# Performance work log

Hardware: AMD Instinct MI355X
Metric: run time of the kernel (lower is better)

Reference implementation:

```python
import jax, jax.numpy as jnp
import numpy as np

N_NODES = 50000
N_EDGES = 600000
IN_FEATS = 128
N_HIDDEN = 128
N_CLASSES = 64


def setup_inputs() -> dict:
    key = jax.random.key(0)
    ks = jax.random.split(key, 10)
    x = jax.random.normal(ks[0], (N_NODES, IN_FEATS), dtype=jnp.float32)
    w = jax.random.uniform(ks[1], (N_EDGES,), dtype=jnp.float32)
    src = jax.random.randint(ks[2], (N_EDGES,), 0, N_NODES, dtype=jnp.int32)
    dst = jax.random.randint(ks[3], (N_EDGES,), 0, N_NODES, dtype=jnp.int32)
    W1 = jax.random.normal(ks[4], (IN_FEATS, N_HIDDEN), dtype=jnp.float32) * 0.05
    b1 = jnp.zeros((N_HIDDEN,), dtype=jnp.float32)
    W2 = jax.random.normal(ks[5], (N_HIDDEN, N_HIDDEN), dtype=jnp.float32) * 0.05
    b2 = jnp.zeros((N_HIDDEN,), dtype=jnp.float32)
    W3 = jax.random.normal(ks[6], (N_HIDDEN, N_CLASSES), dtype=jnp.float32) * 0.05
    b3 = jnp.zeros((N_CLASSES,), dtype=jnp.float32)
    return {"x": x, "w": w, "src": src, "dst": dst,
            "W1": W1, "b1": b1, "W2": W2, "b2": b2, "W3": W3, "b3": b3}


def _graph_conv(h, Wl, bl, w, src, dst, n_nodes):
    # dense linear transform
    h = h @ Wl + bl  # [N, d_out]
    # u_mul_e: gather source features, scale by edge weight
    m = h[src] * w[:, None]  # [E, d_out]
    # sum aggregation into destination nodes
    return jax.ops.segment_sum(m, dst, num_segments=n_nodes)  # [N, d_out]


def reference(x, w, src, dst, W1, b1, W2, b2, W3, b3):
    n = x.shape[0]
    h = jax.nn.relu(_graph_conv(x, W1, b1, w, src, dst, n))
    h = jax.nn.relu(_graph_conv(h, W2, b2, w, src, dst, n))
    return _graph_conv(h, W3, b3, w, src, dst, n)
```

## Files before the change

### kernel.cpp

```cpp
#include <hip/hip_runtime.h>


typedef __attribute__((ext_vector_type(8))) short short8;
typedef __attribute__((ext_vector_type(4))) float float4v;

constexpr int CAP  = 48;
constexpr int CPAD = 16;

__device__ inline unsigned bf16_rne(float f) {
    unsigned u = __float_as_uint(f);
    return (u + 0x7FFF + ((u >> 16) & 1)) >> 16;
}
__device__ inline float bf_lo(unsigned t) { return __uint_as_float(t << 16); }
__device__ inline float bf_hi(unsigned t) { return __uint_as_float(t & 0xFFFF0000u); }

__device__ inline void wprep_one(const float* __restrict__ Wm, int M, int tt,
                                 unsigned short* __restrict__ WfH,
                                 unsigned short* __restrict__ WfL) {
    const int FT = M / 16;
    int lane = tt & 63;
    int ft   = (tt >> 6) % FT;
    int ks   = tt / (64 * FT);
    int n     = ft * 16 + (lane & 15);
    int kbase = ks * 32 + (lane >> 4) * 8;
    #pragma unroll
    for (int j = 0; j < 8; j++) {
        float wv = Wm[(size_t)(kbase + j) * M + n];
        unsigned hb = bf16_rne(wv);
        float wh = __uint_as_float(hb << 16);
        unsigned lb = bf16_rne(wv - wh);
        WfH[(size_t)tt * 8 + j] = (unsigned short)hb;
        WfL[(size_t)tt * 8 + j] = (unsigned short)lb;
    }
}

__global__ void prep_kernel(const float* __restrict__ W1, const float* __restrict__ W2,
                            const float* __restrict__ W3,
                            unsigned short* WfH1, unsigned short* WfL1,
                            unsigned short* WfH2, unsigned short* WfL2,
                            unsigned short* WfH3, unsigned short* WfL3,
                            int* __restrict__ countsP, int N) {
    int t = blockIdx.x * blockDim.x + threadIdx.x;
    if (t < 2048)       wprep_one(W1, 128, t,        WfH1, WfL1);
    else if (t < 4096)  wprep_one(W2, 128, t - 2048, WfH2, WfL2);
    else if (t < 5120)  wprep_one(W3,  64, t - 4096, WfH3, WfL3);
    const int total = N * CPAD;
    for (int i = t; i < total; i += gridDim.x * blockDim.x) countsP[i] = 0;
}

__global__ void scatter_v5(const int* __restrict__ src, const int* __restrict__ dst,
                           const float* __restrict__ w, int* __restrict__ countsP,
                           int2* __restrict__ erec, int E) {
    int e = (blockIdx.x * blockDim.x + threadIdx.x) * 4;
    if (e + 3 < E) {
        int4   d4 = *(const int4*)(dst + e);
        int4   s4 = *(const int4*)(src + e);
        float4 w4 = *(const float4*)(w + e);
        int p0 = atomicAdd(&countsP[d4.x * CPAD], 1);
        int p1 = atomicAdd(&countsP[d4.y * CPAD], 1);
        int p2 = atomicAdd(&countsP[d4.z * CPAD], 1);
        int p3 = atomicAdd(&countsP[d4.w * CPAD], 1);
        if (p0 < CAP) erec[(size_t)d4.x * CAP + p0] = (int2){s4.x, __float_as_int(w4.x)};
        if (p1 < CAP) erec[(size_t)d4.y * CAP + p1] = (int2){s4.y, __float_as_int(w4.y)};
        if (p2 < CAP) erec[(size_t)d4.z * CAP + p2] = (int2){s4.z, __float_as_int(w4.z)};
        if (p3 < CAP) erec[(size_t)d4.w * CAP + p3] = (int2){s4.w, __float_as_int(w4.w)};
    } else {
        for (; e < E; e++) {
            int d = dst[e];
            int p = atomicAdd(&countsP[d * CPAD], 1);
            if (p < CAP) erec[(size_t)d * CAP + p] = (int2){src[e], __float_as_int(w[e])};
        }
    }
}

template <int M>
__global__ __launch_bounds__(256) void gemm_kernel(const float* __restrict__ H,
                                                   const unsigned short* __restrict__ WfH,
                                                   const unsigned short* __restrict__ WfL,
                                                   const float* __restrict__ bias,
                                                   unsigned short* __restrict__ T, int N) {
    const int K  = 128;
    const int KP = K + 4;
    const int FT = M / 16;
    __shared__ float Hs[64 * KP];

    const int node0 = blockIdx.x * 64;
    for (int i = threadIdx.x; i < 64 * (K / 4); i += 256) {
        int r = i / (K / 4), c = i % (K / 4);
        int node = node0 + r;
        float4 hv = {0, 0, 0, 0};
        if (node < N) hv = ((const float4*)(H + (size_t)node * K))[c];
        *(float4*)(Hs + r * KP + c * 4) = hv;
    }
    __syncthreads();

    const int wave = threadIdx.x >> 6;
    const int lane = threadIdx.x & 63;
    const int row  = lane & 15;
    const int ksub = (lane >> 4) * 8;
    const float* hrow = Hs + (wave * 16 + row) * KP;

    float4v acc[FT];
    #pragma unroll
    for (int ft = 0; ft < FT; ft++) acc[ft] = (float4v){0.f, 0.f, 0.f, 0.f};

    #pragma unroll
    for (int ks = 0; ks < 4; ks++) {
        const float* ap = hrow + ks * 32 + ksub;
        float4 a0 = *(const float4*)(ap);
        float4 a1 = *(const float4*)(ap + 4);
        float av[8] = {a0.x, a0.y, a0.z, a0.w, a1.x, a1.y, a1.z, a1.w};
        short8 ah, al;
        #pragma unroll
        for (int j = 0; j < 8; j++) {
            unsigned hb = bf16_rne(av[j]);
            float fh = __uint_as_float(hb << 16);
            ah[j] = (short)hb;
            al[j] = (short)bf16_rne(av[j] - fh);
        }
        #pragma unroll
        for (int ft = 0; ft < FT; ft++) {
            short8 bh = *(const short8*)(WfH + ((size_t)(ks * FT + ft) * 64 + lane) * 8);
            short8 bl = *(const short8*)(WfL + ((size_t)(ks * FT + ft) * 64 + lane) * 8);
            acc[ft] = __builtin_amdgcn_mfma_f32_16x16x32_bf16(ah, bh, acc[ft], 0, 0, 0);
            acc[ft] = __builtin_amdgcn_mfma_f32_16x16x32_bf16(al, bh, acc[ft], 0, 0, 0);
            acc[ft] = __builtin_amdgcn_mfma_f32_16x16x32_bf16(ah, bl, acc[ft], 0, 0, 0);
        }
    }

    const int col   = lane & 15;
    const int rbase = (lane >> 4) * 4;
    #pragma unroll
    for (int ft = 0; ft < FT; ft++) {
        int feat = ft * 16 + col;
        float bv = bias[feat];
        #pragma unroll
        for (int r = 0; r < 4; r++) {
            int node = node0 + wave * 16 + rbase + r;
            if (node < N)
                T[(size_t)node * M + feat] = (unsigned short)bf16_rne(acc[ft][r] + bv);
        }
    }
}

template <int M>
__global__ __launch_bounds__(256) void gemm_bf_kernel(const unsigned short* __restrict__ Hb,
                                                      const unsigned short* __restrict__ WfH,
                                                      const unsigned short* __restrict__ WfL,
                                                      const float* __restrict__ bias,
                                                      unsigned short* __restrict__ T, int N) {
    const int FT = M / 16;
    const int wave = threadIdx.x >> 6;
    const int lane = threadIdx.x & 63;
    const int row  = lane & 15;
    const int ksub = (lane >> 4) * 8;
    const int node0 = blockIdx.x * 64;
    int nodeA = node0 + wave * 16 + row;
    const unsigned short* hp = Hb + (size_t)(nodeA < N ? nodeA : N - 1) * 128;

    float4v acc[FT];
    #pragma unroll
    for (int ft = 0; ft < FT; ft++) acc[ft] = (float4v){0.f, 0.f, 0.f, 0.f};

    #pragma unroll
    for (int ks = 0; ks < 4; ks++) {
        short8 ah = *(const short8*)(hp + ks * 32 + ksub);
        #pragma unroll
        for (int ft = 0; ft < FT; ft++) {
            short8 bh = *(const short8*)(WfH + ((size_t)(ks * FT + ft) * 64 + lane) * 8);
            short8 bl = *(const short8*)(WfL + ((size_t)(ks * FT + ft) * 64 + lane) * 8);
            acc[ft] = __builtin_amdgcn_mfma_f32_16x16x32_bf16(ah, bh, acc[ft], 0, 0, 0);
            acc[ft] = __builtin_amdgcn_mfma_f32_16x16x32_bf16(ah, bl, acc[ft], 0, 0, 0);
        }
    }

    const int col   = lane & 15;
    const int rbase = (lane >> 4) * 4;
    #pragma unroll
    for (int ft = 0; ft < FT; ft++) {
        int feat = ft * 16 + col;
        float bv = bias[feat];
        #pragma unroll
        for (int r = 0; r < 4; r++) {
            int node = node0 + wave * 16 + rbase + r;
            if (node < N)
                T[(size_t)node * M + feat] = (unsigned short)bf16_rne(acc[ft][r] + bv);
        }
    }
}

__global__ void agg128_bf(const unsigned short* __restrict__ Tin,
                          const int* __restrict__ countsP,
                          const int2* __restrict__ erec,
                          unsigned short* __restrict__ Hb, int N) {
    const int wid  = threadIdx.x >> 6;
    const int lane = threadIdx.x & 63;
    const int v = blockIdx.x * 4 + wid;
    if (v >= N) return;
    const int c = min(countsP[v * CPAD], CAP);
    const int q  = lane >> 4;
    const int fo = (lane & 15) * 8;
    float a0 = 0, a1 = 0, a2 = 0, a3 = 0, a4 = 0, a5 = 0, a6 = 0, a7 = 0;
    if (c > 0) {
        const int2* eb = erec + (size_t)v * CAP;
        for (int i = 0; i < c; i += 16) {
            #pragma unroll
            for (int u = 0; u < 4; u++) {
                int idx = i + u * 4 + q;
                float wv = 0.f;
                int cl = idx < c ? idx : c - 1;
                int2 r = eb[cl];
                if (idx < c) wv = __int_as_float(r.y);
                uint4 t = *(const uint4*)(Tin + (size_t)r.x * 128 + fo);
                a0 = fmaf(wv, bf_lo(t.x), a0); a1 = fmaf(wv, bf_hi(t.x), a1);
                a2 = fmaf(wv, bf_lo(t.y), a2); a3 = fmaf(wv, bf_hi(t.y), a3);
                a4 = fmaf(wv, bf_lo(t.z), a4); a5 = fmaf(wv, bf_hi(t.z), a5);
                a6 = fmaf(wv, bf_lo(t.w), a6); a7 = fmaf(wv, bf_hi(t.w), a7);
            }
        }
        a0 += __shfl_xor(a0, 32); a1 += __shfl_xor(a1, 32);
        a2 += __shfl_xor(a2, 32); a3 += __shfl_xor(a3, 32);
        a4 += __shfl_xor(a4, 32); a5 += __shfl_xor(a5, 32);
        a6 += __shfl_xor(a6, 32); a7 += __shfl_xor(a7, 32);
        a0 += __shfl_xor(a0, 16); a1 += __shfl_xor(a1, 16);
        a2 += __shfl_xor(a2, 16); a3 += __shfl_xor(a3, 16);
        a4 += __shfl_xor(a4, 16); a5 += __shfl_xor(a5, 16);
        a6 += __shfl_xor(a6, 16); a7 += __shfl_xor(a7, 16);
    }
    if (lane < 16) {
        float av[8] = {fmaxf(a0, 0.f), fmaxf(a1, 0.f), fmaxf(a2, 0.f), fmaxf(a3, 0.f),
                       fmaxf(a4, 0.f), fmaxf(a5, 0.f), fmaxf(a6, 0.f), fmaxf(a7, 0.f)};
        short8 o;
        #pragma unroll
        for (int j = 0; j < 8; j++) o[j] = (short)bf16_rne(av[j]);
        *(short8*)(Hb + (size_t)v * 128 + fo) = o;
    }
}

__global__ void agg_final_v4(const unsigned short* __restrict__ Tin,
                             const int* __restrict__ countsP,
                             const int2* __restrict__ erec,
                             float* __restrict__ OUT, int N) {
    const int wid  = threadIdx.x >> 6;
    const int lane = threadIdx.x & 63;
    const int v = blockIdx.x * 4 + wid;
    if (v >= N) return;
    const int c = min(countsP[v * CPAD], CAP);
    const int o8 = lane >> 3;
    const int fo = (lane & 7) * 8;
    float a0 = 0, a1 = 0, a2 = 0, a3 = 0, a4 = 0, a5 = 0, a6 = 0, a7 = 0;
    if (c > 0) {
        const int2* eb = erec + (size_t)v * CAP;
        for (int i = 0; i < c; i += 16) {
            #pragma unroll
            for (int u = 0; u < 2; u++) {
                int idx = i + u * 8 + o8;
                float wv = 0.f;
                int cl = idx < c ? idx : c - 1;
                int2 r = eb[cl];
                if (idx < c) wv = __int_as_float(r.y);
                uint4 t = *(const uint4*)(Tin + (size_t)r.x * 64 + fo);
                a0 = fmaf(wv, bf_lo(t.x), a0); a1 = fmaf(wv, bf_hi(t.x), a1);
                a2 = fmaf(wv, bf_lo(t.y), a2); a3 = fmaf(wv, bf_hi(t.y), a3);
                a4 = fmaf(wv, bf_lo(t.z), a4); a5 = fmaf(wv, bf_hi(t.z), a5);
                a6 = fmaf(wv, bf_lo(t.w), a6); a7 = fmaf(wv, bf_hi(t.w), a7);
            }
        }
        a0 += __shfl_xor(a0, 32); a1 += __shfl_xor(a1, 32);
        a2 += __shfl_xor(a2, 32); a3 += __shfl_xor(a3, 32);
        a4 += __shfl_xor(a4, 32); a5 += __shfl_xor(a5, 32);
        a6 += __shfl_xor(a6, 32); a7 += __shfl_xor(a7, 32);
        a0 += __shfl_xor(a0, 16); a1 += __shfl_xor(a1, 16);
        a2 += __shfl_xor(a2, 16); a3 += __shfl_xor(a3, 16);
        a4 += __shfl_xor(a4, 16); a5 += __shfl_xor(a5, 16);
        a6 += __shfl_xor(a6, 16); a7 += __shfl_xor(a7, 16);
        a0 += __shfl_xor(a0, 8);  a1 += __shfl_xor(a1, 8);
        a2 += __shfl_xor(a2, 8);  a3 += __shfl_xor(a3, 8);
        a4 += __shfl_xor(a4, 8);  a5 += __shfl_xor(a5, 8);
        a6 += __shfl_xor(a6, 8);  a7 += __shfl_xor(a7, 8);
    }
    if (lane < 8) {
        float4 o0 = {a0, a1, a2, a3};
        float4 o1 = {a4, a5, a6, a7};
        float* op = OUT + (size_t)v * 64 + fo;
        *(float4*)(op)     = o0;
        *(float4*)(op + 4) = o1;
    }
}

extern "C" void kernel_launch(void* const* d_in, const int* in_sizes, int n_in,
                              void* d_out, int out_size, void* d_ws, size_t ws_size,
                              hipStream_t stream) {
    const float* x   = (const float*)d_in[0];
    const float* w   = (const float*)d_in[1];
    const int*   src = (const int*)d_in[2];
    const int*   dst = (const int*)d_in[3];
    const float* W1  = (const float*)d_in[4];
    const float* b1  = (const float*)d_in[5];
    const float* W2  = (const float*)d_in[6];
    const float* b2  = (const float*)d_in[7];
    const float* W3  = (const float*)d_in[8];
    const float* b3  = (const float*)d_in[9];
    const int N = in_sizes[0] / 128;
    const int E = in_sizes[1];

    unsigned short* Tbf  = (unsigned short*)d_ws;
    unsigned short* Hbf  = Tbf + (size_t)N * 128;
    int2* erec     = (int2*)(Hbf + (size_t)N * 128);
    int*  countsP  = (int*)(erec + (size_t)N * CAP);
    size_t off = (size_t)(countsP + (size_t)N * CPAD - (int*)d_ws);
    off = (off + 3) & ~(size_t)3;
    unsigned short* WfH1 = (unsigned short*)((int*)d_ws + off);
    unsigned short* WfL1 = WfH1 + 128 * 128;
    unsigned short* WfH2 = WfL1 + 128 * 128;
    unsigned short* WfL2 = WfH2 + 128 * 128;
    unsigned short* WfH3 = WfL2 + 128 * 128;
    unsigned short* WfL3 = WfH3 + 128 * 64;

    const int GB = (N + 63) / 64;
    const int AB = (N + 3) / 4;

    prep_kernel<<<96, 256, 0, stream>>>(W1, W2, W3, WfH1, WfL1, WfH2, WfL2,
                                        WfH3, WfL3, countsP, N);
    gemm_kernel<128><<<GB, 256, 0, stream>>>(x, WfH1, WfL1, b1, Tbf, N);
    scatter_v5<<<(E / 4 + 255) / 256, 256, 0, stream>>>(src, dst, w, countsP, erec, E);
    agg128_bf<<<AB, 256, 0, stream>>>(Tbf, countsP, erec, Hbf, N);
    gemm_bf_kernel<128><<<GB, 256, 0, stream>>>(Hbf, WfH2, WfL2, b2, Tbf, N);
    agg128_bf<<<AB, 256, 0, stream>>>(Tbf, countsP, erec, Hbf, N);
    gemm_bf_kernel<64><<<GB, 256, 0, stream>>>(Hbf, WfH3, WfL3, b3, Tbf, N);
    agg_final_v4<<<AB, 256, 0, stream>>>(Tbf, countsP, erec, (float*)d_out, N);
}
```

Before: 242.0 us.

## Fuse edge scatter into layer-1 GEMM launch and prefetch edge records in aggregation

Merges the edge-bucketing scatter and the first dense GEMM into one launch, with the first SB blocks doing the scatter and the rest doing the GEMM, so the two independent stages overlap and one launch is saved. The aggregation kernels now load the first batch of edge records before reading the count and prefetch the next batch during accumulation, so the gather no longer waits on the record load. The count-zeroing loop only clears the used slot of each padded counter. Prefetching reads padded slots past the count that are never used, and the fused kernel mixes two very different block workloads.

After: 236.5 us. 2.3% less time.

```diff
diff --git a/kernel.cpp b/kernel.cpp
--- a/kernel.cpp
+++ b/kernel.cpp
@@ -44,47 +44,47 @@
     if (t < 2048)       wprep_one(W1, 128, t,        WfH1, WfL1);
     else if (t < 4096)  wprep_one(W2, 128, t - 2048, WfH2, WfL2);
     else if (t < 5120)  wprep_one(W3,  64, t - 4096, WfH3, WfL3);
-    const int total = N * CPAD;
-    for (int i = t; i < total; i += gridDim.x * blockDim.x) countsP[i] = 0;
-}
-
-__global__ void scatter_v5(const int* __restrict__ src, const int* __restrict__ dst,
-                           const float* __restrict__ w, int* __restrict__ countsP,
-                           int2* __restrict__ erec, int E) {
-    int e = (blockIdx.x * blockDim.x + threadIdx.x) * 4;
-    if (e + 3 < E) {
-        int4   d4 = *(const int4*)(dst + e);
-        int4   s4 = *(const int4*)(src + e);
-        float4 w4 = *(const float4*)(w + e);
-        int p0 = atomicAdd(&countsP[d4.x * CPAD], 1);
-        int p1 = atomicAdd(&countsP[d4.y * CPAD], 1);
-        int p2 = atomicAdd(&countsP[d4.z * CPAD], 1);
-        int p3 = atomicAdd(&countsP[d4.w * CPAD], 1);
-        if (p0 < CAP) erec[(size_t)d4.x * CAP + p0] = (int2){s4.x, __float_as_int(w4.x)};
-        if (p1 < CAP) erec[(size_t)d4.y * CAP + p1] = (int2){s4.y, __float_as_int(w4.y)};
-        if (p2 < CAP) erec[(size_t)d4.z * CAP + p2] = (int2){s4.z, __float_as_int(w4.z)};
-        if (p3 < CAP) erec[(size_t)d4.w * CAP + p3] = (int2){s4.w, __float_as_int(w4.w)};
-    } else {
-        for (; e < E; e++) {
-            int d = dst[e];
-            int p = atomicAdd(&countsP[d * CPAD], 1);
-            if (p < CAP) erec[(size_t)d * CAP + p] = (int2){src[e], __float_as_int(w[e])};
-        }
-    }
-}
-
-template <int M>
-__global__ __launch_bounds__(256) void gemm_kernel(const float* __restrict__ H,
-                                                   const unsigned short* __restrict__ WfH,
-                                                   const unsigned short* __restrict__ WfL,
-                                                   const float* __restrict__ bias,
-                                                   unsigned short* __restrict__ T, int N) {
+    for (int i = t; i < N; i += gridDim.x * blockDim.x) countsP[i * CPAD] = 0;
+}
+
+__global__ __launch_bounds__(256) void l1_fused(
+        const float* __restrict__ H,
+        const unsigned short* __restrict__ WfH, const unsigned short* __restrict__ WfL,
+        const float* __restrict__ bias, unsigned short* __restrict__ T,
+        const int* __restrict__ src, const int* __restrict__ dst,
+        const float* __restrict__ w, int* __restrict__ countsP,
+        int2* __restrict__ erec, int N, int E, int SB) {
     const int K  = 128;
     const int KP = K + 4;
+    const int M  = 128;
     const int FT = M / 16;
     __shared__ float Hs[64 * KP];
 
-    const int node0 = blockIdx.x * 64;
+    if ((int)blockIdx.x < SB) {
+        int e = (blockIdx.x * 256 + threadIdx.x) * 4;
+        if (e + 3 < E) {
+            int4   d4 = *(const int4*)(dst + e);
+            int4   s4 = *(const int4*)(src + e);
+            float4 w4 = *(const float4*)(w + e);
+            int p0 = atomicAdd(&countsP[d4.x * CPAD], 1);
+            int p1 = atomicAdd(&countsP[d4.y * CPAD], 1);
+            int p2 = atomicAdd(&countsP[d4.z * CPAD], 1);
+            int p3 = atomicAdd(&countsP[d4.w * CPAD], 1);
+            if (p0 < CAP) erec[(size_t)d4.x * CAP + p0] = (int2){s4.x, __float_as_int(w4.x)};
+            if (p1 < CAP) erec[(size_t)d4.y * CAP + p1] = (int2){s4.y, __float_as_int(w4.y)};
+            if (p2 < CAP) erec[(size_t)d4.z * CAP + p2] = (int2){s4.z, __float_as_int(w4.z)};
+            if (p3 < CAP) erec[(size_t)d4.w * CAP + p3] = (int2){s4.w, __float_as_int(w4.w)};
+        } else {
+            for (; e < E; e++) {
+                int d = dst[e];
+                int p = atomicAdd(&countsP[d * CPAD], 1);
+                if (p < CAP) erec[(size_t)d * CAP + p] = (int2){src[e], __float_as_int(w[e])};
+            }
+        }
+        return;
+    }
+
+    const int node0 = (blockIdx.x - SB) * 64;
     for (int i = threadIdx.x; i < 64 * (K / 4); i += 256) {
         int r = i / (K / 4), c = i % (K / 4);
         int node = node0 + r;
@@ -197,36 +197,48 @@
     const int lane = threadIdx.x & 63;
     const int v = blockIdx.x * 4 + wid;
     if (v >= N) return;
-    const int c = min(countsP[v * CPAD], CAP);
     const int q  = lane >> 4;
     const int fo = (lane & 15) * 8;
+    const int2* eb = erec + (size_t)v * CAP;
+
+    int   rx[4]; float wv[4];
+    #pragma unroll
+    for (int u = 0; u < 4; u++) {
+        int2 r = eb[u * 4 + q];
+        rx[u] = r.x; wv[u] = __int_as_float(r.y);
+    }
+    const int c = min(countsP[v * CPAD], CAP);
+
     float a0 = 0, a1 = 0, a2 = 0, a3 = 0, a4 = 0, a5 = 0, a6 = 0, a7 = 0;
-    if (c > 0) {
-        const int2* eb = erec + (size_t)v * CAP;
-        for (int i = 0; i < c; i += 16) {
+    for (int i = 0; i < c; i += 16) {
+        #pragma unroll
+        for (int u = 0; u < 4; u++) {
+            int idx = i + u * 4 + q;
+            if (idx < c) {
+                uint4 t = *(const uint4*)(Tin + (size_t)rx[u] * 128 + fo);
+                float wu = wv[u];
+                a0 = fmaf(wu, bf_lo(t.x), a0); a1 = fmaf(wu, bf_hi(t.x), a1);
+                a2 = fmaf(wu, bf_lo(t.y), a2); a3 = fmaf(wu, bf_hi(t.y), a3);
+                a4 = fmaf(wu, bf_lo(t.z), a4); a5 = fmaf(wu, bf_hi(t.z), a5);
+                a6 = fmaf(wu, bf_lo(t.w), a6); a7 = fmaf(wu, bf_hi(t.w), a7);
+            }
+        }
+        if (i + 16 < c) {
             #pragma unroll
             for (int u = 0; u < 4; u++) {
-                int idx = i + u * 4 + q;
-                float wv = 0.f;
-                int cl = idx < c ? idx : c - 1;
-                int2 r = eb[cl];
-                if (idx < c) wv = __int_as_float(r.y);
-                uint4 t = *(const uint4*)(Tin + (size_t)r.x * 128 + fo);
-                a0 = fmaf(wv, bf_lo(t.x), a0); a1 = fmaf(wv, bf_hi(t.x), a1);
-                a2 = fmaf(wv, bf_lo(t.y), a2); a3 = fmaf(wv, bf_hi(t.y), a3);
-                a4 = fmaf(wv, bf_lo(t.z), a4); a5 = fmaf(wv, bf_hi(t.z), a5);
-                a6 = fmaf(wv, bf_lo(t.w), a6); a7 = fmaf(wv, bf_hi(t.w), a7);
-            }
-        }
-        a0 += __shfl_xor(a0, 32); a1 += __shfl_xor(a1, 32);
-        a2 += __shfl_xor(a2, 32); a3 += __shfl_xor(a3, 32);
-        a4 += __shfl_xor(a4, 32); a5 += __shfl_xor(a5, 32);
-        a6 += __shfl_xor(a6, 32); a7 += __shfl_xor(a7, 32);
-        a0 += __shfl_xor(a0, 16); a1 += __shfl_xor(a1, 16);
-        a2 += __shfl_xor(a2, 16); a3 += __shfl_xor(a3, 16);
-        a4 += __shfl_xor(a4, 16); a5 += __shfl_xor(a5, 16);
-        a6 += __shfl_xor(a6, 16); a7 += __shfl_xor(a7, 16);
-    }
+                int2 r = eb[i + 16 + u * 4 + q];
+                rx[u] = r.x; wv[u] = __int_as_float(r.y);
+            }
+        }
+    }
+    a0 += __shfl_xor(a0, 32); a1 += __shfl_xor(a1, 32);
+    a2 += __shfl_xor(a2, 32); a3 += __shfl_xor(a3, 32);
+    a4 += __shfl_xor(a4, 32); a5 += __shfl_xor(a5, 32);
+    a6 += __shfl_xor(a6, 32); a7 += __shfl_xor(a7, 32);
+    a0 += __shfl_xor(a0, 16); a1 += __shfl_xor(a1, 16);
+    a2 += __shfl_xor(a2, 16); a3 += __shfl_xor(a3, 16);
+    a4 += __shfl_xor(a4, 16); a5 += __shfl_xor(a5, 16);
+    a6 += __shfl_xor(a6, 16); a7 += __shfl_xor(a7, 16);
     if (lane < 16) {
         float av[8] = {fmaxf(a0, 0.f), fmaxf(a1, 0.f), fmaxf(a2, 0.f), fmaxf(a3, 0.f),
                        fmaxf(a4, 0.f), fmaxf(a5, 0.f), fmaxf(a6, 0.f), fmaxf(a7, 0.f)};
@@ -245,40 +257,52 @@
     const int lane = threadIdx.x & 63;
     const int v = blockIdx.x * 4 + wid;
     if (v >= N) return;
-    const int c = min(countsP[v * CPAD], CAP);
     const int o8 = lane >> 3;
     const int fo = (lane & 7) * 8;
+    const int2* eb = erec + (size_t)v * CAP;
+
+    int   rx[2]; float wv[2];
+    #pragma unroll
+    for (int u = 0; u < 2; u++) {
+        int2 r = eb[u * 8 + o8];
+        rx[u] = r.x; wv[u] = __int_as_float(r.y);
+    }
+    const int c = min(countsP[v * CPAD], CAP);
+
     float a0 = 0, a1 = 0, a2 = 0, a3 = 0, a4 = 0, a5 = 0, a6 = 0, a7 = 0;
-    if (c > 0) {
-        const int2* eb = erec + (size_t)v * CAP;
-        for (int i = 0; i < c; i += 16) {
+    for (int i = 0; i < c; i += 16) {
+        #pragma unroll
+        for (int u = 0; u < 2; u++) {
+            int idx = i + u * 8 + o8;
+            if (idx < c) {
+                uint4 t = *(const uint4*)(Tin + (size_t)rx[u] * 64 + fo);
+                float wu = wv[u];
+                a0 = fmaf(wu, bf_lo(t.x), a0); a1 = fmaf(wu, bf_hi(t.x), a1);
+                a2 = fmaf(wu, bf_lo(t.y), a2); a3 = fmaf(wu, bf_hi(t.y), a3);
+                a4 = fmaf(wu, bf_lo(t.z), a4); a5 = fmaf(wu, bf_hi(t.z), a5);
+                a6 = fmaf(wu, bf_lo(t.w), a6); a7 = fmaf(wu, bf_hi(t.w), a7);
+            }
+        }
+        if (i + 16 < c) {
             #pragma unroll
             for (int u = 0; u < 2; u++) {
-                int idx = i + u * 8 + o8;
-                float wv = 0.f;
-                int cl = idx < c ? idx : c - 1;
-                int2 r = eb[cl];
-                if (idx < c) wv = __int_as_float(r.y);
-                uint4 t = *(const uint4*)(Tin + (size_t)r.x * 64 + fo);
-                a0 = fmaf(wv, bf_lo(t.x), a0); a1 = fmaf(wv, bf_hi(t.x), a1);
-                a2 = fmaf(wv, bf_lo(t.y), a2); a3 = fmaf(wv, bf_hi(t.y), a3);
-                a4 = fmaf(wv, bf_lo(t.z), a4); a5 = fmaf(wv, bf_hi(t.z), a5);
-                a6 = fmaf(wv, bf_lo(t.w), a6); a7 = fmaf(wv, bf_hi(t.w), a7);
-            }
-        }
-        a0 += __shfl_xor(a0, 32); a1 += __shfl_xor(a1, 32);
-        a2 += __shfl_xor(a2, 32); a3 += __shfl_xor(a3, 32);
-        a4 += __shfl_xor(a4, 32); a5 += __shfl_xor(a5, 32);
-        a6 += __shfl_xor(a6, 32); a7 += __shfl_xor(a7, 32);
-        a0 += __shfl_xor(a0, 16); a1 += __shfl_xor(a1, 16);
-        a2 += __shfl_xor(a2, 16); a3 += __shfl_xor(a3, 16);
-        a4 += __shfl_xor(a4, 16); a5 += __shfl_xor(a5, 16);
-        a6 += __shfl_xor(a6, 16); a7 += __shfl_xor(a7, 16);
-        a0 += __shfl_xor(a0, 8);  a1 += __shfl_xor(a1, 8);
-        a2 += __shfl_xor(a2, 8);  a3 += __shfl_xor(a3, 8);
-        a4 += __shfl_xor(a4, 8);  a5 += __shfl_xor(a5, 8);
-        a6 += __shfl_xor(a6, 8);  a7 += __shfl_xor(a7, 8);
-    }
+                int2 r = eb[i + 16 + u * 8 + o8];
+                rx[u] = r.x; wv[u] = __int_as_float(r.y);
+            }
+        }
+    }
+    a0 += __shfl_xor(a0, 32); a1 += __shfl_xor(a1, 32);
+    a2 += __shfl_xor(a2, 32); a3 += __shfl_xor(a3, 32);
+    a4 += __shfl_xor(a4, 32); a5 += __shfl_xor(a5, 32);
+    a6 += __shfl_xor(a6, 32); a7 += __shfl_xor(a7, 32);
+    a0 += __shfl_xor(a0, 16); a1 += __shfl_xor(a1, 16);
+    a2 += __shfl_xor(a2, 16); a3 += __shfl_xor(a3, 16);
+    a4 += __shfl_xor(a4, 16); a5 += __shfl_xor(a5, 16);
+    a6 += __shfl_xor(a6, 16); a7 += __shfl_xor(a7, 16);
+    a0 += __shfl_xor(a0, 8);  a1 += __shfl_xor(a1, 8);
+    a2 += __shfl_xor(a2, 8);  a3 += __shfl_xor(a3, 8);
+    a4 += __shfl_xor(a4, 8);  a5 += __shfl_xor(a5, 8);
+    a6 += __shfl_xor(a6, 8);  a7 += __shfl_xor(a7, 8);
     if (lane < 8) {
         float4 o0 = {a0, a1, a2, a3};
         float4 o1 = {a4, a5, a6, a7};
@@ -318,12 +342,13 @@
     unsigned short* WfL3 = WfH3 + 128 * 64;
 
     const int GB = (N + 63) / 64;
+    const int SB = (E / 4 + 255) / 256;
     const int AB = (N + 3) / 4;
 
     prep_kernel<<<96, 256, 0, stream>>>(W1, W2, W3, WfH1, WfL1, WfH2, WfL2,
                                         WfH3, WfL3, countsP, N);
-    gemm_kernel<128><<<GB, 256, 0, stream>>>(x, WfH1, WfL1, b1, Tbf, N);
-    scatter_v5<<<(E / 4 + 255) / 256, 256, 0, stream>>>(src, dst, w, countsP, erec, E);
+    l1_fused<<<SB + GB, 256, 0, stream>>>(x, WfH1, WfL1, b1, Tbf,
+                                          src, dst, w, countsP, erec, N, E, SB);
     agg128_bf<<<AB, 256, 0, stream>>>(Tbf, countsP, erec, Hbf, N);
     gemm_bf_kernel<128><<<GB, 256, 0, stream>>>(Hbf, WfH2, WfL2, b2, Tbf, N);
     agg128_bf<<<AB, 256, 0, stream>>>(Tbf, countsP, erec, Hbf, N);
```
